# Kernel tuning notes

Measured on AMD Instinct MI355X. Metric: run time of the kernel, lower is better.

## Reference

```python
import jax, jax.numpy as jnp
import numpy as np

H, N, SEQ = 256, 64, 4096

def setup_inputs() -> dict:
    key = jax.random.key(0)
    kA, kB, kC, kdt = jax.random.split(key, 4)
    W = jax.random.normal(kA, (H, N, N), dtype=jnp.float32)
    # Hurwitz (stable) A: skew-symmetric part minus 0.5*I, like HiPPO-style stable transitions
    A = 0.5 * (W - jnp.swapaxes(W, -1, -2)) - 0.5 * jnp.eye(N, dtype=jnp.float32)
    B = jax.random.normal(kB, (H, N), dtype=jnp.float32)
    C = jax.random.normal(kC, (H, N), dtype=jnp.float32)
    # log_dt around log(0.01), matching typical S4 timescale init
    log_dt = jax.random.normal(kdt, (H,), dtype=jnp.float32) * 0.5 + jnp.log(0.01)
    return {"A": A, "B": B, "C": C, "log_dt": log_dt, "L": SEQ}

def _bilinear(dt, A, B):
    # dt: (H,), A: (H,N,N), B: (H,N)
    n = A.shape[-1]
    I = jnp.eye(n, dtype=A.dtype)
    A_back = I - (dt[:, None, None] / 2) * A   # (H,N,N)
    A_fwd = I + (dt[:, None, None] / 2) * A    # (H,N,N)
    dA = jnp.linalg.solve(A_back, A_fwd)                       # (H,N,N)
    dB = dt[:, None] * jnp.linalg.solve(A_back, B[..., None])[..., 0]  # (H,N)
    return dA, dB

def _krylov(L, dA, dB, C):
    # K[h, l] = C[h] @ dA[h]^l @ dB[h], computed by squaring/doubling
    x = dB[..., None]  # (H, N, 1)
    A_ = dA
    while x.shape[-1] < L:
        x2 = jnp.einsum('hmn,hnl->hml', A_, x)  # apply current power
        x = jnp.concatenate([x, x2], axis=-1)
        if x.shape[-1] < L:
            A_ = jnp.einsum('hmn,hnk->hmk', A_, A_)  # square the power
    x = x[..., :L]  # (H, N, L)
    return jnp.einsum('hn,hnl->hl', C, x)  # (H, L)

def reference(A, B, C, log_dt, L):
    dt = jnp.exp(log_dt)
    dA, dB = _bilinear(dt, A, B)
    return _krylov(L, dA, dB, C)
```

## Files before the change

### kernel.cpp

```cpp
#include <hip/hip_runtime.h>

constexpr int STRU = 68;

typedef short v8s __attribute__((ext_vector_type(8)));
typedef float v4f __attribute__((ext_vector_type(4)));

__device__ __forceinline__ unsigned packhl(float x) {
    unsigned xb = __builtin_bit_cast(unsigned, x);
    unsigned hb = xb & 0xffff0000u;
    float lof = x - __builtin_bit_cast(float, hb);
    unsigned lb = __builtin_bit_cast(unsigned, lof) + 0x8000u;
    return __builtin_amdgcn_perm(xb, lb, 0x07060302u);
}

__device__ __forceinline__ float unpackf(unsigned v) {
    float h = __builtin_bit_cast(float, v & 0xffff0000u);
    float l = __builtin_bit_cast(float, v << 16);
    return h + l;
}

__device__ __forceinline__ void load_frag(const unsigned* p, v8s& hi, v8s& lo) {
    uint4 a = *(const uint4*)p;
    uint4 b = *(const uint4*)(p + 4);
    uint4 hw, lw;
    hw.x = __builtin_amdgcn_perm(a.y, a.x, 0x07060302u);
    hw.y = __builtin_amdgcn_perm(a.w, a.z, 0x07060302u);
    hw.z = __builtin_amdgcn_perm(b.y, b.x, 0x07060302u);
    hw.w = __builtin_amdgcn_perm(b.w, b.z, 0x07060302u);
    lw.x = __builtin_amdgcn_perm(a.y, a.x, 0x05040100u);
    lw.y = __builtin_amdgcn_perm(a.w, a.z, 0x05040100u);
    lw.z = __builtin_amdgcn_perm(b.y, b.x, 0x05040100u);
    lw.w = __builtin_amdgcn_perm(b.w, b.z, 0x05040100u);
    hi = __builtin_bit_cast(v8s, hw);
    lo = __builtin_bit_cast(v8s, lw);
}

#define MFMA __builtin_amdgcn_mfma_f32_16x16x32_bf16

template<int MODE>
__device__ __forceinline__ void mm64(const unsigned* __restrict__ P,
                                     const unsigned* __restrict__ Q,
                                     unsigned* D, unsigned* DT, float* G,
                                     const unsigned* R, float ca, float cb,
                                     int tid) {
    const int lane = tid & 63, w = tid >> 6;
    const int nh = lane & 15, qh = lane >> 4;
    const int tr = w >> 1, tc0 = (w & 1) << 1;
    v4f acc[2] = {v4f{0,0,0,0}, v4f{0,0,0,0}};
    #pragma unroll
    for (int kk = 0; kk < 2; ++kk) {
        const int kc = kk * 32 + qh * 8;
        v8s ph, pl, q0h, q0l, q1h, q1l;
        load_frag(P + (tr * 16 + nh) * STRU + kc, ph, pl);
        load_frag(Q + (tc0 * 16 + nh) * STRU + kc, q0h, q0l);
        load_frag(Q + ((tc0 + 1) * 16 + nh) * STRU + kc, q1h, q1l);
        acc[0] = MFMA(ph, q0h, acc[0], 0, 0, 0);
        acc[0] = MFMA(ph, q0l, acc[0], 0, 0, 0);
        acc[0] = MFMA(pl, q0h, acc[0], 0, 0, 0);
        acc[1] = MFMA(ph, q1h, acc[1], 0, 0, 0);
        acc[1] = MFMA(ph, q1l, acc[1], 0, 0, 0);
        acc[1] = MFMA(pl, q1h, acc[1], 0, 0, 0);
    }
    const int row0 = tr * 16 + qh * 4;
    #pragma unroll
    for (int c = 0; c < 2; ++c) {
        const int col = (tc0 + c) * 16 + nh;
        if constexpr (MODE == 2) {
            #pragma unroll
            for (int e = 0; e < 4; ++e) G[(row0 + e) * 64 + col] = acc[c][e];
        } else if constexpr (MODE == 0) {
            #pragma unroll
            for (int e = 0; e < 4; ++e)
                D[(row0 + e) * STRU + col] = packhl(acc[c][e]);
        } else if constexpr (MODE == 1) {
            #pragma unroll
            for (int e = 0; e < 4; ++e) {
                float v = acc[c][e] + ((row0 + e) == col ? 1.0f : 0.0f);
                D[(row0 + e) * STRU + col] = packhl(v);
            }
        } else if constexpr (MODE == 3) {
            uint4 tp;
            #pragma unroll
            for (int e = 0; e < 4; ++e) {
                unsigned pk = packhl(acc[c][e]);
                D[(row0 + e) * STRU + col] = pk;
                ((unsigned*)&tp)[e] = pk;
            }
            *(uint4*)&DT[col * STRU + row0] = tp;
        } else if constexpr (MODE == 4) {
            #pragma unroll
            for (int e = 0; e < 4; ++e) {
                float dv = ca * acc[c][e];
                float dg = ((row0 + e) == col) ? 1.0f : 0.0f;
                D[(row0 + e) * STRU + col]  = packhl(dv);
                DT[(row0 + e) * STRU + col] = packhl(dv + dg);
            }
        } else if constexpr (MODE == 5) {
            #pragma unroll
            for (int e = 0; e < 4; ++e) {
                float t  = unpackf(R[(row0 + e) * STRU + col]);
                float dg = ((row0 + e) == col) ? 1.0f : 0.0f;
                float base = ca * t - dg;
                float sv   = cb * acc[c][e];
                D[(row0 + e) * STRU + col]  = packhl(base + sv);
                DT[(row0 + e) * STRU + col] = packhl(base - sv);
            }
        }
    }
}

__device__ __forceinline__ void dbl64(unsigned* Xt, const unsigned* M, int k, int tid) {
    const int lane = tid & 63, w = tid >> 6;
    const int nh = lane & 15, qh = lane >> 4;
    const int nt = (k + 15) >> 4;
    if (w < 4 * nt) {
        const int t = w >> 2, cb = w & 3;
        v4f acc = {0, 0, 0, 0};
        #pragma unroll
        for (int kk = 0; kk < 2; ++kk) {
            const int kc = kk * 32 + qh * 8;
            v8s ph, pl, mh, ml;
            load_frag(Xt + (t * 16 + nh) * STRU + kc, ph, pl);
            load_frag(M + (cb * 16 + nh) * STRU + kc, mh, ml);
            acc = MFMA(ph, mh, acc, 0, 0, 0);
            acc = MFMA(ph, ml, acc, 0, 0, 0);
            acc = MFMA(pl, mh, acc, 0, 0, 0);
        }
        #pragma unroll
        for (int e = 0; e < 4; ++e) {
            const int j = t * 16 + qh * 4 + e;
            if (j < k) Xt[(k + j) * STRU + cb * 16 + nh] = packhl(acc[e]);
        }
    }
}

__launch_bounds__(512)
__global__ void krylov_kernel(const float* __restrict__ A,
                              const float* __restrict__ Bv,
                              const float* __restrict__ Cv,
                              const float* __restrict__ logdt,
                              float* __restrict__ out)
{
    const int h    = blockIdx.x;
    const int tid  = threadIdx.x;
    const int lane = tid & 63;
    const int w    = tid >> 6;

    __shared__ __align__(16) unsigned SM[6][64 * STRU];
    __shared__ float Bl[64];

    const float dt = expf(logdt[h]);
    const float c  = 0.5f * dt;
    const float al = 1.0f + 0.5f * c;
    const float sd = -(c * c) / (al * al);
    const float c1 = 2.0f / al;
    const float c2 = 2.0f * c / (al * al);

    const float* Ah = A + (size_t)h * 4096;

    for (int idx = tid; idx < 1024; idx += 512) {
        const int r = idx >> 4, c0 = (idx & 15) * 4;
        float4 v = *(const float4*)(Ah + idx * 4);
        if (r == c0 + 0) v.x += 0.5f;
        if (r == c0 + 1) v.y += 0.5f;
        if (r == c0 + 2) v.z += 0.5f;
        if (r == c0 + 3) v.w += 0.5f;
        uint4 pk = make_uint4(packhl(v.x), packhl(v.y), packhl(v.z), packhl(v.w));
        *(uint4*)&SM[0][r * STRU + c0] = pk;
    }
    if (tid < 64) Bl[tid] = Bv[h * 64 + tid];
    else if (tid < 128) SM[5][tid - 64] = packhl(Cv[h * 64 + (tid - 64)]);
    __syncthreads();

    mm64<4>(SM[0], SM[0], SM[1], SM[2], nullptr, nullptr, sd, 0.f, tid);
    __syncthreads();
    mm64<1>(SM[1], SM[2], SM[3], nullptr, nullptr, nullptr, 0.f, 0.f, tid);
    __syncthreads();
    mm64<1>(SM[1], SM[3], SM[2], nullptr, nullptr, nullptr, 0.f, 0.f, tid);
    __syncthreads();
    mm64<1>(SM[1], SM[2], SM[3], nullptr, nullptr, nullptr, 0.f, 0.f, tid);
    __syncthreads();
    mm64<5>(SM[0], SM[3], SM[2], SM[1], nullptr, SM[3], c1, c2, tid);
    __syncthreads();

    if (w == 0) {
        const unsigned* Xr = SM[2] + lane * STRU;
        float acc = 0.0f;
        #pragma unroll
        for (int m4 = 0; m4 < 16; ++m4) {
            uint4 xv = *(const uint4*)(Xr + 4 * m4);
            float4 b4 = *(const float4*)&Bl[4 * m4];
            acc += unpackf(xv.x) * b4.x + unpackf(xv.y) * b4.y
                 + unpackf(xv.z) * b4.z + unpackf(xv.w) * b4.w;
        }
        SM[4][lane] = packhl(c * (acc + Bl[lane]));
    }
    __syncthreads();

    unsigned *bX = SM[2], *bXT = SM[1], *bN = SM[0], *bNT = SM[3];
    #pragma unroll 1
    for (int s = 0; s < 6; ++s) {
        mm64<3>(bX, bXT, bN, bNT, nullptr, nullptr, 0.f, 0.f, tid);
        dbl64(SM[4], bX, 1 << s, tid);
        __syncthreads();
        unsigned* t0 = bX;  bX  = bN;  bN  = t0;
        t0 = bXT; bXT = bNT; bNT = t0;
    }

    #pragma unroll 1
    for (int s = 0; s < 6; ++s) {
        if (s < 5) mm64<3>(bX, bXT, bN, bNT, nullptr, nullptr, 0.f, 0.f, tid);
        dbl64(SM[5], bXT, 1 << s, tid);
        __syncthreads();
        if (s < 5) {
            unsigned* t0 = bX;  bX  = bN;  bN  = t0;
            t0 = bXT; bXT = bNT; bNT = t0;
        }
    }

    mm64<2>(SM[5], SM[4], nullptr, nullptr, out + (size_t)h * 4096, nullptr,
            0.f, 0.f, tid);
}

extern "C" void kernel_launch(void* const* d_in, const int* in_sizes, int n_in,
                              void* d_out, int out_size, void* d_ws, size_t ws_size,
                              hipStream_t stream) {
    const float* A  = (const float*)d_in[0];
    const float* B  = (const float*)d_in[1];
    const float* C  = (const float*)d_in[2];
    const float* ld = (const float*)d_in[3];
    float* out = (float*)d_out;
    const int H = in_sizes[3];
    krylov_kernel<<<H, 512, 0, stream>>>(A, B, C, ld, out);
}
```

Before: 78.79 us.

## Double block size to 1024 threads with one MFMA tile per wave

The block grows from 512 to 1024 threads (16 waves). Each wave in the 64x64 matmul helper now computes a single 16x16 output tile instead of two, and the A-matrix load loop collapses to one float4 per thread. The aim is to shorten each serial matmul step and hide more MFMA and LDS latency in what is a long dependent chain with one block per CU. In exchange, barriers now cover twice as many waves, per-wave register headroom shrinks, and fragment loads are duplicated across more waves.

```diff
diff --git a/kernel.cpp b/kernel.cpp
--- a/kernel.cpp
+++ b/kernel.cpp
@@ -45,66 +45,59 @@
                                      int tid) {
     const int lane = tid & 63, w = tid >> 6;
     const int nh = lane & 15, qh = lane >> 4;
-    const int tr = w >> 1, tc0 = (w & 1) << 1;
-    v4f acc[2] = {v4f{0,0,0,0}, v4f{0,0,0,0}};
+    const int tr = w >> 2, tc = w & 3;
+    v4f acc = {0, 0, 0, 0};
     #pragma unroll
     for (int kk = 0; kk < 2; ++kk) {
         const int kc = kk * 32 + qh * 8;
-        v8s ph, pl, q0h, q0l, q1h, q1l;
+        v8s ph, pl, bh, bl;
         load_frag(P + (tr * 16 + nh) * STRU + kc, ph, pl);
-        load_frag(Q + (tc0 * 16 + nh) * STRU + kc, q0h, q0l);
-        load_frag(Q + ((tc0 + 1) * 16 + nh) * STRU + kc, q1h, q1l);
-        acc[0] = MFMA(ph, q0h, acc[0], 0, 0, 0);
-        acc[0] = MFMA(ph, q0l, acc[0], 0, 0, 0);
-        acc[0] = MFMA(pl, q0h, acc[0], 0, 0, 0);
-        acc[1] = MFMA(ph, q1h, acc[1], 0, 0, 0);
-        acc[1] = MFMA(ph, q1l, acc[1], 0, 0, 0);
-        acc[1] = MFMA(pl, q1h, acc[1], 0, 0, 0);
+        load_frag(Q + (tc * 16 + nh) * STRU + kc, bh, bl);
+        acc = MFMA(ph, bh, acc, 0, 0, 0);
+        acc = MFMA(ph, bl, acc, 0, 0, 0);
+        acc = MFMA(pl, bh, acc, 0, 0, 0);
     }
     const int row0 = tr * 16 + qh * 4;
-    #pragma unroll
-    for (int c = 0; c < 2; ++c) {
-        const int col = (tc0 + c) * 16 + nh;
-        if constexpr (MODE == 2) {
-            #pragma unroll
-            for (int e = 0; e < 4; ++e) G[(row0 + e) * 64 + col] = acc[c][e];
-        } else if constexpr (MODE == 0) {
-            #pragma unroll
-            for (int e = 0; e < 4; ++e)
-                D[(row0 + e) * STRU + col] = packhl(acc[c][e]);
-        } else if constexpr (MODE == 1) {
-            #pragma unroll
-            for (int e = 0; e < 4; ++e) {
-                float v = acc[c][e] + ((row0 + e) == col ? 1.0f : 0.0f);
-                D[(row0 + e) * STRU + col] = packhl(v);
-            }
-        } else if constexpr (MODE == 3) {
-            uint4 tp;
-            #pragma unroll
-            for (int e = 0; e < 4; ++e) {
-                unsigned pk = packhl(acc[c][e]);
-                D[(row0 + e) * STRU + col] = pk;
-                ((unsigned*)&tp)[e] = pk;
-            }
-            *(uint4*)&DT[col * STRU + row0] = tp;
-        } else if constexpr (MODE == 4) {
-            #pragma unroll
-            for (int e = 0; e < 4; ++e) {
-                float dv = ca * acc[c][e];
-                float dg = ((row0 + e) == col) ? 1.0f : 0.0f;
-                D[(row0 + e) * STRU + col]  = packhl(dv);
-                DT[(row0 + e) * STRU + col] = packhl(dv + dg);
-            }
-        } else if constexpr (MODE == 5) {
-            #pragma unroll
-            for (int e = 0; e < 4; ++e) {
-                float t  = unpackf(R[(row0 + e) * STRU + col]);
-                float dg = ((row0 + e) == col) ? 1.0f : 0.0f;
-                float base = ca * t - dg;
-                float sv   = cb * acc[c][e];
-                D[(row0 + e) * STRU + col]  = packhl(base + sv);
-                DT[(row0 + e) * STRU + col] = packhl(base - sv);
-            }
+    const int col  = tc * 16 + nh;
+    if constexpr (MODE == 2) {
+        #pragma unroll
+        for (int e = 0; e < 4; ++e) G[(row0 + e) * 64 + col] = acc[e];
+    } else if constexpr (MODE == 0) {
+        #pragma unroll
+        for (int e = 0; e < 4; ++e)
+            D[(row0 + e) * STRU + col] = packhl(acc[e]);
+    } else if constexpr (MODE == 1) {
+        #pragma unroll
+        for (int e = 0; e < 4; ++e) {
+            float v = acc[e] + ((row0 + e) == col ? 1.0f : 0.0f);
+            D[(row0 + e) * STRU + col] = packhl(v);
+        }
+    } else if constexpr (MODE == 3) {
+        uint4 tp;
+        #pragma unroll
+        for (int e = 0; e < 4; ++e) {
+            unsigned pk = packhl(acc[e]);
+            D[(row0 + e) * STRU + col] = pk;
+            ((unsigned*)&tp)[e] = pk;
+        }
+        *(uint4*)&DT[col * STRU + row0] = tp;
+    } else if constexpr (MODE == 4) {
+        #pragma unroll
+        for (int e = 0; e < 4; ++e) {
+            float dv = ca * acc[e];
+            float dg = ((row0 + e) == col) ? 1.0f : 0.0f;
+            D[(row0 + e) * STRU + col]  = packhl(dv);
+            DT[(row0 + e) * STRU + col] = packhl(dv + dg);
+        }
+    } else if constexpr (MODE == 5) {
+        #pragma unroll
+        for (int e = 0; e < 4; ++e) {
+            float t  = unpackf(R[(row0 + e) * STRU + col]);
+            float dg = ((row0 + e) == col) ? 1.0f : 0.0f;
+            float base = ca * t - dg;
+            float sv   = cb * acc[e];
+            D[(row0 + e) * STRU + col]  = packhl(base + sv);
+            DT[(row0 + e) * STRU + col] = packhl(base - sv);
         }
     }
 }
@@ -134,7 +127,7 @@
     }
 }
 
-__launch_bounds__(512)
+__launch_bounds__(1024)
 __global__ void krylov_kernel(const float* __restrict__ A,
                               const float* __restrict__ Bv,
                               const float* __restrict__ Cv,
@@ -158,9 +151,9 @@
 
     const float* Ah = A + (size_t)h * 4096;
 
-    for (int idx = tid; idx < 1024; idx += 512) {
-        const int r = idx >> 4, c0 = (idx & 15) * 4;
-        float4 v = *(const float4*)(Ah + idx * 4);
+    {
+        const int r = tid >> 4, c0 = (tid & 15) * 4;
+        float4 v = *(const float4*)(Ah + tid * 4);
         if (r == c0 + 0) v.x += 0.5f;
         if (r == c0 + 1) v.y += 0.5f;
         if (r == c0 + 2) v.z += 0.5f;
@@ -231,5 +224,5 @@
     const float* ld = (const float*)d_in[3];
     float* out = (float*)d_out;
     const int H = in_sizes[3];
-    krylov_kernel<<<H, 512, 0, stream>>>(A, B, C, ld, out);
-}
+    krylov_kernel<<<H, 1024, 0, stream>>>(A, B, C, ld, out);
+}
```

Measured after the change: 79.01 us. About the same (+0.3%).

## Pack two heads per 1024-thread block and cut LDS buffers via in-place updates

Applied to the files above, without the earlier changes.

Each block now processes two heads with 512 threads each. The squaring and doubling loops compute into registers, synchronise, then write back in place, so four LDS buffers per head suffice instead of six. The Neumann-series setup is also reordered so the matrix square is reused. The aim is fewer blocks than CUs (128 for 256 heads) with larger blocks, plus lower LDS footprint, at the cost of an extra barrier per step and half the block count, which may leave CUs idle.

```diff
diff --git a/kernel.cpp b/kernel.cpp
--- a/kernel.cpp
+++ b/kernel.cpp
@@ -37,16 +37,14 @@
 
 #define MFMA __builtin_amdgcn_mfma_f32_16x16x32_bf16
 
-template<int MODE>
-__device__ __forceinline__ void mm64(const unsigned* __restrict__ P,
-                                     const unsigned* __restrict__ Q,
-                                     unsigned* D, unsigned* DT, float* G,
-                                     const unsigned* R, float ca, float cb,
-                                     int tid) {
-    const int lane = tid & 63, w = tid >> 6;
+__device__ __forceinline__ void mm_compute(const unsigned* __restrict__ P,
+                                           const unsigned* __restrict__ Q,
+                                           int htid, v4f acc[2]) {
+    const int lane = htid & 63, w = htid >> 6;
     const int nh = lane & 15, qh = lane >> 4;
     const int tr = w >> 1, tc0 = (w & 1) << 1;
-    v4f acc[2] = {v4f{0,0,0,0}, v4f{0,0,0,0}};
+    acc[0] = v4f{0, 0, 0, 0};
+    acc[1] = v4f{0, 0, 0, 0};
     #pragma unroll
     for (int kk = 0; kk < 2; ++kk) {
         const int kc = kk * 32 + qh * 8;
@@ -61,6 +59,16 @@
         acc[1] = MFMA(ph, q1l, acc[1], 0, 0, 0);
         acc[1] = MFMA(pl, q1h, acc[1], 0, 0, 0);
     }
+}
+
+template<int MODE>
+__device__ __forceinline__ void mm_write(const v4f acc[2],
+                                         unsigned* D, unsigned* DT, float* G,
+                                         const unsigned* R, float ca, float cb,
+                                         int htid) {
+    const int lane = htid & 63, w = htid >> 6;
+    const int nh = lane & 15, qh = lane >> 4;
+    const int tr = w >> 1, tc0 = (w & 1) << 1;
     const int row0 = tr * 16 + qh * 4;
     #pragma unroll
     for (int c = 0; c < 2; ++c) {
@@ -109,45 +117,60 @@
     }
 }
 
-__device__ __forceinline__ void dbl64(unsigned* Xt, const unsigned* M, int k, int tid) {
-    const int lane = tid & 63, w = tid >> 6;
+__device__ __forceinline__ bool dbl_compute(const unsigned* __restrict__ Xt,
+                                            const unsigned* __restrict__ M,
+                                            int k, int htid, v4f& acc) {
+    const int lane = htid & 63, w = htid >> 6;
     const int nh = lane & 15, qh = lane >> 4;
     const int nt = (k + 15) >> 4;
-    if (w < 4 * nt) {
-        const int t = w >> 2, cb = w & 3;
-        v4f acc = {0, 0, 0, 0};
-        #pragma unroll
-        for (int kk = 0; kk < 2; ++kk) {
-            const int kc = kk * 32 + qh * 8;
-            v8s ph, pl, mh, ml;
-            load_frag(Xt + (t * 16 + nh) * STRU + kc, ph, pl);
-            load_frag(M + (cb * 16 + nh) * STRU + kc, mh, ml);
-            acc = MFMA(ph, mh, acc, 0, 0, 0);
-            acc = MFMA(ph, ml, acc, 0, 0, 0);
-            acc = MFMA(pl, mh, acc, 0, 0, 0);
-        }
-        #pragma unroll
-        for (int e = 0; e < 4; ++e) {
-            const int j = t * 16 + qh * 4 + e;
-            if (j < k) Xt[(k + j) * STRU + cb * 16 + nh] = packhl(acc[e]);
-        }
-    }
-}
-
-__launch_bounds__(512)
+    if (w >= 4 * nt) return false;
+    const int t = w >> 2, cb = w & 3;
+    acc = v4f{0, 0, 0, 0};
+    #pragma unroll
+    for (int kk = 0; kk < 2; ++kk) {
+        const int kc = kk * 32 + qh * 8;
+        v8s ph, pl, mh, ml;
+        load_frag(Xt + (t * 16 + nh) * STRU + kc, ph, pl);
+        load_frag(M + (cb * 16 + nh) * STRU + kc, mh, ml);
+        acc = MFMA(ph, mh, acc, 0, 0, 0);
+        acc = MFMA(ph, ml, acc, 0, 0, 0);
+        acc = MFMA(pl, mh, acc, 0, 0, 0);
+    }
+    return true;
+}
+
+__device__ __forceinline__ void dbl_write(const v4f& acc, unsigned* Xt, int k,
+                                          int htid) {
+    const int lane = htid & 63, w = htid >> 6;
+    const int nh = lane & 15, qh = lane >> 4;
+    const int t = w >> 2, cb = w & 3;
+    #pragma unroll
+    for (int e = 0; e < 4; ++e) {
+        const int j = t * 16 + qh * 4 + e;
+        if (j < k) Xt[(k + j) * STRU + cb * 16 + nh] = packhl(acc[e]);
+    }
+}
+
+__launch_bounds__(1024)
 __global__ void krylov_kernel(const float* __restrict__ A,
                               const float* __restrict__ Bv,
                               const float* __restrict__ Cv,
                               const float* __restrict__ logdt,
                               float* __restrict__ out)
 {
-    const int h    = blockIdx.x;
     const int tid  = threadIdx.x;
-    const int lane = tid & 63;
-    const int w    = tid >> 6;
-
-    __shared__ __align__(16) unsigned SM[6][64 * STRU];
-    __shared__ float Bl[64];
+    const int hd   = tid >> 9;
+    const int htid = tid & 511;
+    const int h    = blockIdx.x * 2 + hd;
+    const int lane = htid & 63;
+
+    __shared__ __align__(16) unsigned SM[8][64 * STRU];
+    __shared__ float Bl[2][64];
+
+    unsigned* b0 = SM[hd * 4 + 0];
+    unsigned* b1 = SM[hd * 4 + 1];
+    unsigned* b2 = SM[hd * 4 + 2];
+    unsigned* b3 = SM[hd * 4 + 3];
 
     const float dt = expf(logdt[h]);
     const float c  = 0.5f * dt;
@@ -158,7 +181,7 @@
 
     const float* Ah = A + (size_t)h * 4096;
 
-    for (int idx = tid; idx < 1024; idx += 512) {
+    for (int idx = htid; idx < 1024; idx += 512) {
         const int r = idx >> 4, c0 = (idx & 15) * 4;
         float4 v = *(const float4*)(Ah + idx * 4);
         if (r == c0 + 0) v.x += 0.5f;
@@ -166,60 +189,72 @@
         if (r == c0 + 2) v.z += 0.5f;
         if (r == c0 + 3) v.w += 0.5f;
         uint4 pk = make_uint4(packhl(v.x), packhl(v.y), packhl(v.z), packhl(v.w));
-        *(uint4*)&SM[0][r * STRU + c0] = pk;
-    }
-    if (tid < 64) Bl[tid] = Bv[h * 64 + tid];
-    else if (tid < 128) SM[5][tid - 64] = packhl(Cv[h * 64 + (tid - 64)]);
-    __syncthreads();
-
-    mm64<4>(SM[0], SM[0], SM[1], SM[2], nullptr, nullptr, sd, 0.f, tid);
-    __syncthreads();
-    mm64<1>(SM[1], SM[2], SM[3], nullptr, nullptr, nullptr, 0.f, 0.f, tid);
-    __syncthreads();
-    mm64<1>(SM[1], SM[3], SM[2], nullptr, nullptr, nullptr, 0.f, 0.f, tid);
-    __syncthreads();
-    mm64<1>(SM[1], SM[2], SM[3], nullptr, nullptr, nullptr, 0.f, 0.f, tid);
-    __syncthreads();
-    mm64<5>(SM[0], SM[3], SM[2], SM[1], nullptr, SM[3], c1, c2, tid);
-    __syncthreads();
-
-    if (w == 0) {
-        const unsigned* Xr = SM[2] + lane * STRU;
-        float acc = 0.0f;
+        *(uint4*)&b0[r * STRU + c0] = pk;
+    }
+    if (htid < 64) Bl[hd][htid] = Bv[h * 64 + htid];
+    __syncthreads();
+
+    v4f acc[2];
+
+    mm_compute(b0, b0, htid, acc);
+    mm_write<4>(acc, b1, b2, nullptr, nullptr, sd, 0.f, htid);
+    __syncthreads();
+    mm_compute(b1, b1, htid, acc);
+    mm_write<1>(acc, b3, nullptr, nullptr, nullptr, 0.f, 0.f, htid);
+    __syncthreads();
+    mm_compute(b2, b3, htid, acc);
+    mm_write<0>(acc, b1, nullptr, nullptr, nullptr, 0.f, 0.f, htid);
+    __syncthreads();
+    mm_compute(b0, b1, htid, acc);
+    mm_write<5>(acc, b2, b3, nullptr, b1, c1, c2, htid);
+    __syncthreads();
+
+    if ((htid >> 6) == 0) {
+        const unsigned* Xr = b2 + lane * STRU;
+        float a2 = 0.0f;
         #pragma unroll
         for (int m4 = 0; m4 < 16; ++m4) {
             uint4 xv = *(const uint4*)(Xr + 4 * m4);
-            float4 b4 = *(const float4*)&Bl[4 * m4];
-            acc += unpackf(xv.x) * b4.x + unpackf(xv.y) * b4.y
-                 + unpackf(xv.z) * b4.z + unpackf(xv.w) * b4.w;
+            float4 b4 = *(const float4*)&Bl[hd][4 * m4];
+            a2 += unpackf(xv.x) * b4.x + unpackf(xv.y) * b4.y
+                + unpackf(xv.z) * b4.z + unpackf(xv.w) * b4.w;
         }
-        SM[4][lane] = packhl(c * (acc + Bl[lane]));
-    }
-    __syncthreads();
-
-    unsigned *bX = SM[2], *bXT = SM[1], *bN = SM[0], *bNT = SM[3];
+        b1[lane] = packhl(c * (a2 + Bl[hd][lane]));
+    } else if (htid < 128) {
+        b0[htid - 64] = packhl(Cv[h * 64 + (htid - 64)]);
+    }
+    __syncthreads();
+
     #pragma unroll 1
     for (int s = 0; s < 6; ++s) {
-        mm64<3>(bX, bXT, bN, bNT, nullptr, nullptr, 0.f, 0.f, tid);
-        dbl64(SM[4], bX, 1 << s, tid);
-        __syncthreads();
-        unsigned* t0 = bX;  bX  = bN;  bN  = t0;
-        t0 = bXT; bXT = bNT; bNT = t0;
+        const int k = 1 << s;
+        mm_compute(b2, b3, htid, acc);
+        v4f da; const bool dv = dbl_compute(b1, b2, k, htid, da);
+        __syncthreads();
+        mm_write<3>(acc, b2, b3, nullptr, nullptr, 0.f, 0.f, htid);
+        if (dv) dbl_write(da, b1, k, htid);
+        __syncthreads();
     }
 
     #pragma unroll 1
-    for (int s = 0; s < 6; ++s) {
-        if (s < 5) mm64<3>(bX, bXT, bN, bNT, nullptr, nullptr, 0.f, 0.f, tid);
-        dbl64(SM[5], bXT, 1 << s, tid);
-        __syncthreads();
-        if (s < 5) {
-            unsigned* t0 = bX;  bX  = bN;  bN  = t0;
-            t0 = bXT; bXT = bNT; bNT = t0;
-        }
-    }
-
-    mm64<2>(SM[5], SM[4], nullptr, nullptr, out + (size_t)h * 4096, nullptr,
-            0.f, 0.f, tid);
+    for (int s = 0; s < 5; ++s) {
+        const int k = 1 << s;
+        mm_compute(b2, b3, htid, acc);
+        v4f da; const bool dv = dbl_compute(b0, b3, k, htid, da);
+        __syncthreads();
+        mm_write<3>(acc, b2, b3, nullptr, nullptr, 0.f, 0.f, htid);
+        if (dv) dbl_write(da, b0, k, htid);
+        __syncthreads();
+    }
+    {
+        v4f da; const bool dv = dbl_compute(b0, b3, 32, htid, da);
+        if (dv) dbl_write(da, b0, 32, htid);
+        __syncthreads();
+    }
+
+    mm_compute(b0, b1, htid, acc);
+    mm_write<2>(acc, nullptr, nullptr, out + (size_t)h * 4096, nullptr,
+                0.f, 0.f, htid);
 }
 
 extern "C" void kernel_launch(void* const* d_in, const int* in_sizes, int n_in,
@@ -231,5 +266,5 @@
     const float* ld = (const float*)d_in[3];
     float* out = (float*)d_out;
     const int H = in_sizes[3];
-    krylov_kernel<<<H, 512, 0, stream>>>(A, B, C, ld, out);
-}
+    krylov_kernel<<<H / 2, 1024, 0, stream>>>(A, B, C, ld, out);
+}
```

After: 89.27 us. +13.3%, slower.
